# Performance work log

Measured on AMD Instinct MI355X. Metric: run time of the kernel, lower is better.

The kernel has to match this reference:

```python
import jax, jax.numpy as jnp
import numpy as np

NUM_HEADS = 16
ROPE_THETA = 10000.0


def _rope(x, pos):
    # x: [B, H, S, d_k], pos: [S]
    d_k = x.shape[-1]
    inv_freq = ROPE_THETA ** (-jnp.arange(0, d_k, 2, dtype=x.dtype) / d_k)  # [d_k/2]
    ang = pos[:, None].astype(x.dtype) * inv_freq[None, :]  # [S, d_k/2]
    cos, sin = jnp.cos(ang), jnp.sin(ang)
    x1 = x[..., 0::2]
    x2 = x[..., 1::2]
    r1 = x1 * cos - x2 * sin
    r2 = x1 * sin + x2 * cos
    return jnp.stack([r1, r2], axis=-1).reshape(x.shape)


def setup_inputs() -> dict:
    key = jax.random.key(0)
    kx, kq, kk, kv = jax.random.split(key, 4)
    B, S, D = 2, 2048, 2048
    scale = 1.0 / np.sqrt(D)
    x = jax.random.normal(kx, (B, S, D), dtype=jnp.float32)
    wq = jax.random.normal(kq, (D, D), dtype=jnp.float32) * scale
    wk = jax.random.normal(kk, (D, D), dtype=jnp.float32) * scale
    wv = jax.random.normal(kv, (D, D), dtype=jnp.float32) * scale
    return {"x": x, "wq": wq, "wk": wk, "wv": wv}


def reference(x, wq, wk, wv):
    B, S, D = x.shape
    H = NUM_HEADS
    d_k = D // H
    # QKV projections (Linear stores weight as [out, in]; y = x @ W^T)
    q = (x @ wq.T).reshape(B, S, H, d_k).transpose(0, 2, 1, 3)  # [B,H,S,dk]
    k = (x @ wk.T).reshape(B, S, H, d_k).transpose(0, 2, 1, 3)
    v = (x @ wv.T).reshape(B, S, H, d_k).transpose(0, 2, 1, 3)
    pos = jnp.arange(S)
    q = _rope(q, pos)
    k = _rope(k, pos)
    scores = jnp.einsum("bhqd,bhkd->bhqk", q, k) / jnp.sqrt(jnp.asarray(d_k, x.dtype))
    causal = jnp.tril(jnp.ones((S, S), dtype=bool))
    scores = jnp.where(causal, scores, jnp.asarray(-1e9, x.dtype))
    attn = jax.nn.softmax(scores, axis=-1)
    out = jnp.einsum("bhqk,bhkd->bhqd", attn, v)  # [B,H,S,dk]
    return out.transpose(0, 2, 1, 3).reshape(B, S, D)
```

## Files before the change

kernel.cpp:

```cpp
#include <hip/hip_runtime.h>
#include <stdint.h>

typedef unsigned short u16;
typedef __bf16 bf16x8 __attribute__((ext_vector_type(8)));
typedef float f32x4 __attribute__((ext_vector_type(4)));
typedef float f32x16 __attribute__((ext_vector_type(16)));

#define NHEADS 16
#define DKH    128
#define SEQ    2048
#define DMODEL 2048
#define NBATCH 2

typedef const __attribute__((address_space(1))) void* gas1_t;
typedef __attribute__((address_space(3))) void* las3_t;

__device__ __forceinline__ void gload_lds16(const void* g, void* l) {
  __builtin_amdgcn_global_load_lds((gas1_t)(uintptr_t)g,
                                   (las3_t)(uint32_t)(uintptr_t)l, 16, 0, 0);
}

__device__ __forceinline__ u16 bf(float f) {
  return __builtin_bit_cast(u16, (__bf16)f);
}

__device__ __forceinline__ uint32_t pk(float lo, float hi) {
  return (uint32_t)bf(lo) | ((uint32_t)bf(hi) << 16);
}

__device__ __forceinline__ float lanebcast(int srclane, float v) {
  return __builtin_bit_cast(float,
      __builtin_amdgcn_ds_bpermute(srclane << 2, __builtin_bit_cast(int, v)));
}

__global__ __launch_bounds__(256) void cvt_all(const float* __restrict__ x,
                                               const float* __restrict__ wq,
                                               const float* __restrict__ wk,
                                               const float* __restrict__ wv,
                                               u16* __restrict__ xb,
                                               u16* __restrict__ wb) {
  int i = (blockIdx.x * 256 + threadIdx.x) * 4;
  const int NX = NBATCH * SEQ * DMODEL;
  const int NW = DMODEL * DMODEL;
  const float* src;
  u16* dst;
  int j;
  if (i < NX) { src = x; dst = xb; j = i; }
  else {
    int k = i - NX;
    int w = k / NW;
    j = k - w * NW;
    src = (w == 0) ? wq : (w == 1) ? wk : wv;
    dst = wb + (size_t)w * NW;
  }
  const float4 v = *(const float4*)(src + j);
  uint2 o;
  o.x = (uint32_t)bf(v.x) | ((uint32_t)bf(v.y) << 16);
  o.y = (uint32_t)bf(v.z) | ((uint32_t)bf(v.w) << 16);
  *(uint2*)(dst + j) = o;
}

__global__ __launch_bounds__(256) void rope_table(float2* __restrict__ tbl) {
  int i = blockIdx.x * 256 + threadIdx.x;
  int s = i >> 6, d2 = i & 63;
  const float kLog2Theta = 13.28771237954945f;
  float inv_freq = exp2f(-(float)d2 * (2.0f / 128.0f) * kLog2Theta);
  float ang = (float)s * inv_freq;
  tbl[i] = make_float2(cosf(ang), sinf(ang));
}

__global__ __launch_bounds__(256, 4) void gemm_qkv(const u16* __restrict__ Abf,
                                                   const u16* __restrict__ Wbf,
                                                   const float2* __restrict__ rope,
                                                   u16* __restrict__ qb,
                                                   u16* __restrict__ kb,
                                                   u16* __restrict__ vtb) {
  __shared__ u16 S[16384];
  u16* As = S;
  u16* Bs = S + 8192;
  const int tid = threadIdx.x;
  const int lane = tid & 63, wid = tid >> 6;
  const int wr = wid >> 1, wc = wid & 1;
  const int blk = blockIdx.x;
  const int m0 = (blk / 48) * 128;
  const int n0 = (blk % 48) * 128;
  const int lrow = lane & 15, lgrp = lane >> 4, lko = lgrp * 8;
  const int rswz = (lrow & 7) << 3;

  const int srow = tid >> 3;
  const int scol = ((tid & 7) * 8) ^ (((tid >> 3) & 7) << 3);

  f32x4 acc[4][4] = {};

  for (int k0 = 0; k0 < DMODEL; k0 += 64) {
    __syncthreads();
#pragma unroll
    for (int c = 0; c < 4; ++c) {
      gload_lds16(Abf + (size_t)(m0 + c * 32 + srow) * DMODEL + k0 + scol,
                  As + (c * 256 + tid) * 8);
      gload_lds16(Wbf + (size_t)(n0 + c * 32 + srow) * DMODEL + k0 + scol,
                  Bs + (c * 256 + tid) * 8);
    }
    __syncthreads();
#pragma unroll
    for (int kk = 0; kk < 2; ++kk) {
      const int rc = (kk * 32 + lko) ^ rswz;
      bf16x8 a[4], b[4];
#pragma unroll
      for (int m = 0; m < 4; ++m)
        a[m] = *(const bf16x8*)(As + (wr * 64 + m * 16 + lrow) * 64 + rc);
#pragma unroll
      for (int n = 0; n < 4; ++n)
        b[n] = *(const bf16x8*)(Bs + (wc * 64 + n * 16 + lrow) * 64 + rc);
#pragma unroll
      for (int m = 0; m < 4; ++m)
#pragma unroll
        for (int n = 0; n < 4; ++n)
          acc[m][n] = __builtin_amdgcn_mfma_f32_16x16x32_bf16(a[m], b[n], acc[m][n], 0, 0, 0);
    }
  }

  const int sel = n0 >> 11;
  const float qsc = 0.08838834764831845f * 1.44269504088896341f;

  if (sel != 2) {
#pragma unroll
    for (int m = 0; m < 4; ++m) {
      int grow0 = m0 + wr * 64 + m * 16 + (lgrp << 2);
#pragma unroll
      for (int n = 0; n < 4; ++n) {
        int gcol = n0 + wc * 64 + n * 16 + lrow;
        int within = gcol & 2047;
        int h_ = within >> 7, d_ = within & 127;
#pragma unroll
        for (int j = 0; j < 4; ++j) {
          float v = acc[m][n][j];
          int r = grow0 + j;
          int b_ = r >> 11, s_ = r & 2047;
          int bh = b_ * NHEADS + h_;
          float part = __shfl_xor(v, 1);
          float2 cs2 = rope[s_ * 64 + (d_ >> 1)];
          v = (d_ & 1) ? (part * cs2.y + v * cs2.x) : (v * cs2.x - part * cs2.y);
          if (sel == 0) v *= qsc;
          u16* dq = sel ? kb : qb;
          dq[((size_t)bh * SEQ + s_) * DKH + d_] = bf(v);
        }
      }
    }
  } else {
    __syncthreads();
#pragma unroll
    for (int m = 0; m < 4; ++m) {
      int sl0 = wr * 64 + m * 16 + (lgrp << 2);
#pragma unroll
      for (int n = 0; n < 4; ++n) {
        int dcol = wc * 64 + n * 16 + lrow;
        const int dx = (dcol & 7) << 4;
#pragma unroll
        for (int j = 0; j < 4; ++j)
          S[dcol * 128 + ((sl0 + j) ^ dx)] = bf(acc[m][n][j]);
      }
    }
    __syncthreads();
    const int b_ = m0 >> 11, s0 = m0 & 2047;
    const int h_ = (n0 >> 7) & 15;
    const int bh = b_ * NHEADS + h_;
    const int d = tid >> 1, hf = tid & 1;
    const int dx = (d & 7) << 4;
    u16* grow = vtb + ((size_t)bh * DKH + d) * SEQ + s0 + hf * 64;
#pragma unroll
    for (int g = 0; g < 8; ++g) {
      bf16x8 v8 = *(const bf16x8*)(S + d * 128 + ((hf * 64 + g * 8) ^ dx));
      *(bf16x8*)(grow + g * 8) = v8;
    }
  }
}

__global__ __launch_bounds__(256, 2) void attn_fwd(const u16* __restrict__ qb,
                                                   const u16* __restrict__ kb,
                                                   const u16* __restrict__ vtb,
                                                   float* __restrict__ out) {
  __shared__ u16 Ks[2][64 * 128];
  __shared__ u16 Vs[2][128 * 64];
  const int tid = threadIdx.x, lane = tid & 63, wid = tid >> 6;
  const int blk = blockIdx.x;
  const int r_ = blk & 255, half = blk >> 8;
  const int bh = r_ & 31;
  const int pairidx = r_ >> 5;
  const int chunk = half ? (15 - pairidx) : pairidx;
  const int qln = lane & 31, hi = lane >> 5;
  const int hi4 = hi << 2, hi8 = hi << 3;
  const int kswz = (qln & 15) << 3;
  const int vswz = (qln & 7) << 3;

  const int krow_l = tid >> 4;
  const int kcol = (((tid & 15) ^ (tid >> 4)) << 3);
  const int vrow_l = tid >> 3;
  const int vcol = (((tid & 7) ^ ((tid >> 3) & 7)) << 3);

  const int b_ = bh >> 4, h_ = bh & 15;
  const size_t kbase = (size_t)bh * SEQ;
  const size_t vbase = (size_t)bh * DKH;

#define STAGE_KV(bufi, kv_)                                                  \
  _Pragma("unroll")                                                          \
  for (int c = 0; c < 4; ++c) {                                              \
    gload_lds16(kb + (kbase + (kv_) + c * 16 + krow_l) * DKH + kcol,         \
                &Ks[bufi][(c * 256 + tid) * 8]);                             \
    gload_lds16(vtb + (vbase + c * 32 + vrow_l) * SEQ + (kv_) + vcol,        \
                &Vs[bufi][(c * 256 + tid) * 8]);                             \
  }

  const int q0w = chunk * 128 + wid * 32;
  const int qglob = q0w + qln;

  bf16x8 qa[8];
#pragma unroll
  for (int kd = 0; kd < 8; ++kd)
    qa[kd] = *(const bf16x8*)(qb + (kbase + q0w + qln) * DKH + kd * 16 + hi8);

  f32x16 o[4] = {};
  float mrun = -1e30f, lrun = 0.f;

  const int nt = 2 * chunk + 2;

  STAGE_KV(0, 0);
  __syncthreads();

#pragma unroll 1
  for (int t = 0; t < nt; ++t) {
    const int cur = t & 1;
    if (t + 1 < nt) { STAGE_KV(cur ^ 1, (t + 1) * 64); }
    const int kv0 = t * 64;

    if (kv0 <= q0w + 31) {
      const u16* Kb = &Ks[cur][0];
      const u16* Vb = &Vs[cur][0];

      f32x16 sfv[2] = {};
      __builtin_amdgcn_s_setprio(1);
#pragma unroll
      for (int kd = 0; kd < 8; ++kd)
#pragma unroll
        for (int st = 0; st < 2; ++st) {
          bf16x8 kf = *(const bf16x8*)(Kb + (st * 32 + qln) * 128 +
                                       ((kd * 16 + hi8) ^ kswz));
          sfv[st] = __builtin_amdgcn_mfma_f32_32x32x16_bf16(kf, qa[kd], sfv[st], 0, 0, 0);
        }
      __builtin_amdgcn_s_setprio(0);

      if (kv0 + 63 > q0w) {
#pragma unroll
        for (int st = 0; st < 2; ++st)
#pragma unroll
          for (int r = 0; r < 16; ++r)
            if (kv0 + st * 32 + ((r & 3) + 8 * (r >> 2)) + hi4 > qglob)
              sfv[st][r] = -1e30f;
      }

      float tm[16];
#pragma unroll
      for (int r = 0; r < 16; ++r) tm[r] = fmaxf(sfv[0][r], sfv[1][r]);
#pragma unroll
      for (int r = 0; r < 8; ++r) tm[r] = fmaxf(tm[r], tm[r + 8]);
#pragma unroll
      for (int r = 0; r < 4; ++r) tm[r] = fmaxf(tm[r], tm[r + 4]);
      float m_ = fmaxf(fmaxf(tm[0], tm[1]), fmaxf(tm[2], tm[3]));
      m_ = fmaxf(m_, __shfl_xor(m_, 32));

      if (__any(m_ > mrun + 11.5f)) {
        float mnew = fmaxf(mrun, m_);
        float alpha = __builtin_amdgcn_exp2f(mrun - mnew);
        mrun = mnew;
        lrun *= alpha;
#pragma unroll
        for (int r = 0; r < 16; ++r) {
          float ar = lanebcast((r & 3) + 8 * (r >> 2) + hi4, alpha);
          o[0][r] *= ar; o[1][r] *= ar; o[2][r] *= ar; o[3][r] *= ar;
        }
      }

#pragma unroll
      for (int st = 0; st < 2; ++st)
#pragma unroll
        for (int r = 0; r < 16; ++r)
          sfv[st][r] = __builtin_amdgcn_exp2f(sfv[st][r] - mrun);
      float ts[16];
#pragma unroll
      for (int r = 0; r < 16; ++r) ts[r] = sfv[0][r] + sfv[1][r];
#pragma unroll
      for (int r = 0; r < 8; ++r) ts[r] += ts[r + 8];
#pragma unroll
      for (int r = 0; r < 4; ++r) ts[r] += ts[r + 4];
      float sum = (ts[0] + ts[1]) + (ts[2] + ts[3]);
      sum += __shfl_xor(sum, 32);
      lrun += sum;

      __builtin_amdgcn_s_setprio(1);
#pragma unroll
      for (int ks = 0; ks < 4; ++ks) {
        const int st = ks >> 1, rb = (ks & 1) * 8;
        uint32_t w0 = pk(sfv[st][rb + 0], sfv[st][rb + 1]);
        uint32_t w1 = pk(sfv[st][rb + 2], sfv[st][rb + 3]);
        uint32_t w2 = pk(sfv[st][rb + 4], sfv[st][rb + 5]);
        uint32_t w3 = pk(sfv[st][rb + 6], sfv[st][rb + 7]);
        uint32_t s0 = hi ? w0 : w2, s1 = hi ? w1 : w3;
        uint32_t r0 = (uint32_t)__shfl_xor((int)s0, 32);
        uint32_t r1 = (uint32_t)__shfl_xor((int)s1, 32);
        union { uint32_t u[4]; bf16x8 v; } pa;
        pa.u[0] = hi ? r0 : w0;
        pa.u[1] = hi ? r1 : w1;
        pa.u[2] = hi ? w2 : r0;
        pa.u[3] = hi ? w3 : r1;
#pragma unroll
        for (int d0 = 0; d0 < 4; ++d0) {
          bf16x8 vf = *(const bf16x8*)(Vb + (d0 * 32 + qln) * 64 +
                                       ((ks * 16 + hi8) ^ vswz));
          o[d0] = __builtin_amdgcn_mfma_f32_32x32x16_bf16(pa.v, vf, o[d0], 0, 0, 0);
        }
      }
      __builtin_amdgcn_s_setprio(0);
    }

    __syncthreads();
  }

  float inv = 1.f / lrun;
#pragma unroll
  for (int r = 0; r < 16; ++r) {
    const int qr = (r & 3) + 8 * (r >> 2) + hi4;
    float invr = lanebcast(qr, inv);
    float* op = out + ((size_t)b_ * SEQ + q0w + qr) * DMODEL + h_ * DKH + qln;
    op[0]  = o[0][r] * invr;
    op[32] = o[1][r] * invr;
    op[64] = o[2][r] * invr;
    op[96] = o[3][r] * invr;
  }
#undef STAGE_KV
}

extern "C" void kernel_launch(void* const* d_in, const int* in_sizes, int n_in,
                              void* d_out, int out_size, void* d_ws, size_t ws_size,
                              hipStream_t stream) {
  const float* x  = (const float*)d_in[0];
  const float* wq = (const float*)d_in[1];
  const float* wk = (const float*)d_in[2];
  const float* wv = (const float*)d_in[3];
  float* out = (float*)d_out;
  char* ws = (char*)d_ws;

  u16* xb  = (u16*)(ws);
  u16* wb  = (u16*)(ws + 16777216);
  u16* qb  = (u16*)(ws + 41943040);
  u16* kb  = (u16*)(ws + 58720256);
  u16* vtb = (u16*)(ws + 75497472);

  float2* rope = (float2*)d_out;

  rope_table<<<512, 256, 0, stream>>>(rope);
  cvt_all<<<20480, 256, 0, stream>>>(x, wq, wk, wv, xb, wb);
  gemm_qkv<<<1536, 256, 0, stream>>>(xb, wb, rope, qb, kb, vtb);
  attn_fwd<<<512, 256, 0, stream>>>(qb, kb, vtb, out);
}
```

Before: 191.7 us.

## Single-buffer V in attention to raise occupancy; fuse rope table into convert kernel

The attention kernel drops double buffering of V: V is now staged into one LDS buffer at the start of each tile, overlapping with the QK^T and softmax work, and the next K tile is prefetched after a mid-iteration barrier. This cuts LDS per block from 64KB to 48KB and raises the launch bounds to 3 blocks per CU, aiming for higher occupancy. The cost is an extra barrier per iteration and less time to hide V load latency. Separately, the rope table computation is folded into the convert kernel as extra blocks, removing one kernel launch.

```diff
diff --git a/kernel.cpp b/kernel.cpp
--- a/kernel.cpp
+++ b/kernel.cpp
@@ -38,8 +38,19 @@
                                                const float* __restrict__ wk,
                                                const float* __restrict__ wv,
                                                u16* __restrict__ xb,
-                                               u16* __restrict__ wb) {
-  int i = (blockIdx.x * 256 + threadIdx.x) * 4;
+                                               u16* __restrict__ wb,
+                                               float2* __restrict__ rope) {
+  const int gb = blockIdx.x;
+  if (gb >= 20480) {
+    int i = (gb - 20480) * 256 + threadIdx.x;
+    int s = i >> 6, d2 = i & 63;
+    const float kLog2Theta = 13.28771237954945f;
+    float inv_freq = exp2f(-(float)d2 * (2.0f / 128.0f) * kLog2Theta);
+    float ang = (float)s * inv_freq;
+    rope[i] = make_float2(cosf(ang), sinf(ang));
+    return;
+  }
+  int i = (gb * 256 + threadIdx.x) * 4;
   const int NX = NBATCH * SEQ * DMODEL;
   const int NW = DMODEL * DMODEL;
   const float* src;
@@ -58,15 +69,6 @@
   o.x = (uint32_t)bf(v.x) | ((uint32_t)bf(v.y) << 16);
   o.y = (uint32_t)bf(v.z) | ((uint32_t)bf(v.w) << 16);
   *(uint2*)(dst + j) = o;
-}
-
-__global__ __launch_bounds__(256) void rope_table(float2* __restrict__ tbl) {
-  int i = blockIdx.x * 256 + threadIdx.x;
-  int s = i >> 6, d2 = i & 63;
-  const float kLog2Theta = 13.28771237954945f;
-  float inv_freq = exp2f(-(float)d2 * (2.0f / 128.0f) * kLog2Theta);
-  float ang = (float)s * inv_freq;
-  tbl[i] = make_float2(cosf(ang), sinf(ang));
 }
 
 __global__ __launch_bounds__(256, 4) void gemm_qkv(const u16* __restrict__ Abf,
@@ -176,12 +178,12 @@
   }
 }
 
-__global__ __launch_bounds__(256, 2) void attn_fwd(const u16* __restrict__ qb,
+__global__ __launch_bounds__(256, 3) void attn_fwd(const u16* __restrict__ qb,
                                                    const u16* __restrict__ kb,
                                                    const u16* __restrict__ vtb,
                                                    float* __restrict__ out) {
   __shared__ u16 Ks[2][64 * 128];
-  __shared__ u16 Vs[2][128 * 64];
+  __shared__ u16 Vs[128 * 64];
   const int tid = threadIdx.x, lane = tid & 63, wid = tid >> 6;
   const int blk = blockIdx.x;
   const int r_ = blk & 255, half = blk >> 8;
@@ -202,14 +204,16 @@
   const size_t kbase = (size_t)bh * SEQ;
   const size_t vbase = (size_t)bh * DKH;
 
-#define STAGE_KV(bufi, kv_)                                                  \
+#define STAGE_K(bufi, kv_)                                                   \
   _Pragma("unroll")                                                          \
-  for (int c = 0; c < 4; ++c) {                                              \
+  for (int c = 0; c < 4; ++c)                                                \
     gload_lds16(kb + (kbase + (kv_) + c * 16 + krow_l) * DKH + kcol,         \
-                &Ks[bufi][(c * 256 + tid) * 8]);                             \
+                &Ks[bufi][(c * 256 + tid) * 8]);
+#define STAGE_V(kv_)                                                         \
+  _Pragma("unroll")                                                          \
+  for (int c = 0; c < 4; ++c)                                                \
     gload_lds16(vtb + (vbase + c * 32 + vrow_l) * SEQ + (kv_) + vcol,        \
-                &Vs[bufi][(c * 256 + tid) * 8]);                             \
-  }
+                &Vs[(c * 256 + tid) * 8]);
 
   const int q0w = chunk * 128 + wid * 32;
   const int qglob = q0w + qln;
@@ -224,20 +228,21 @@
 
   const int nt = 2 * chunk + 2;
 
-  STAGE_KV(0, 0);
+  STAGE_K(0, 0);
   __syncthreads();
 
 #pragma unroll 1
   for (int t = 0; t < nt; ++t) {
     const int cur = t & 1;
-    if (t + 1 < nt) { STAGE_KV(cur ^ 1, (t + 1) * 64); }
     const int kv0 = t * 64;
-
-    if (kv0 <= q0w + 31) {
+    const bool active = (kv0 <= q0w + 31);
+
+    STAGE_V(kv0);
+
+    f32x16 sfv[2] = {};
+    if (active) {
       const u16* Kb = &Ks[cur][0];
-      const u16* Vb = &Vs[cur][0];
-
-      f32x16 sfv[2] = {};
+
       __builtin_amdgcn_s_setprio(1);
 #pragma unroll
       for (int kd = 0; kd < 8; ++kd)
@@ -295,7 +300,13 @@
       float sum = (ts[0] + ts[1]) + (ts[2] + ts[3]);
       sum += __shfl_xor(sum, 32);
       lrun += sum;
-
+    }
+
+    __syncthreads();
+
+    if (t + 1 < nt) { STAGE_K(cur ^ 1, (t + 1) * 64); }
+
+    if (active) {
       __builtin_amdgcn_s_setprio(1);
 #pragma unroll
       for (int ks = 0; ks < 4; ++ks) {
@@ -314,7 +325,7 @@
         pa.u[3] = hi ? w3 : r1;
 #pragma unroll
         for (int d0 = 0; d0 < 4; ++d0) {
-          bf16x8 vf = *(const bf16x8*)(Vb + (d0 * 32 + qln) * 64 +
+          bf16x8 vf = *(const bf16x8*)(Vs + (d0 * 32 + qln) * 64 +
                                        ((ks * 16 + hi8) ^ vswz));
           o[d0] = __builtin_amdgcn_mfma_f32_32x32x16_bf16(pa.v, vf, o[d0], 0, 0, 0);
         }
@@ -336,7 +347,8 @@
     op[64] = o[2][r] * invr;
     op[96] = o[3][r] * invr;
   }
-#undef STAGE_KV
+#undef STAGE_K
+#undef STAGE_V
 }
 
 extern "C" void kernel_launch(void* const* d_in, const int* in_sizes, int n_in,
@@ -357,8 +369,7 @@
 
   float2* rope = (float2*)d_out;
 
-  rope_table<<<512, 256, 0, stream>>>(rope);
-  cvt_all<<<20480, 256, 0, stream>>>(x, wq, wk, wv, xb, wb);
+  cvt_all<<<20992, 256, 0, stream>>>(x, wq, wk, wv, xb, wb, rope);
   gemm_qkv<<<1536, 256, 0, stream>>>(xb, wb, rope, qb, kb, vtb);
   attn_fwd<<<512, 256, 0, stream>>>(qb, kb, vtb, out);
 }
```

Result: slower. 219.6 us (+14.6%).
